# Kernel tuning notes

Hardware: AMD Instinct MI355X
Metric: run time of the kernel (lower is better)

The kernel has to match this reference:

```python
import jax, jax.numpy as jnp
import numpy as np

EMBED = 1024
HEADS = 16
HEAD_SIZE = EMBED // HEADS
B, T = 2, 2048
EPS = 1e-5


def layer_norm(x, g, b):
    mu = jnp.mean(x, axis=-1, keepdims=True)
    var = jnp.var(x, axis=-1, keepdims=True)
    return (x - mu) * jax.lax.rsqrt(var + EPS) * g + b


def setup_inputs() -> dict:
    key = jax.random.key(0)
    ks = jax.random.split(key, 12)
    s = 0.02
    return {
        "x": jax.random.normal(ks[0], (B, T, EMBED), jnp.float32),
        "Wq": s * jax.random.normal(ks[1], (EMBED, EMBED), jnp.float32),
        "Wk": s * jax.random.normal(ks[2], (EMBED, EMBED), jnp.float32),
        "Wv": s * jax.random.normal(ks[3], (EMBED, EMBED), jnp.float32),
        "Wo": s * jax.random.normal(ks[4], (EMBED, EMBED), jnp.float32),
        "bo": jnp.zeros((EMBED,), jnp.float32),
        "W1": s * jax.random.normal(ks[5], (EMBED, 4 * EMBED), jnp.float32),
        "b1": jnp.zeros((4 * EMBED,), jnp.float32),
        "W2": s * jax.random.normal(ks[6], (4 * EMBED, EMBED), jnp.float32),
        "b2": jnp.zeros((EMBED,), jnp.float32),
        "ln1_g": jnp.ones((EMBED,), jnp.float32),
        "ln1_b": jnp.zeros((EMBED,), jnp.float32),
        "ln2_g": jnp.ones((EMBED,), jnp.float32),
        "ln2_b": jnp.zeros((EMBED,), jnp.float32),
    }


def reference(x, Wq, Wk, Wv, Wo, bo, W1, b1, W2, b2, ln1_g, ln1_b, ln2_g, ln2_b):
    # --- multi-head causal self-attention on ln1(x) ---
    h = layer_norm(x, ln1_g, ln1_b)                      # [B,T,D]
    q = (h @ Wq).reshape(B, T, HEADS, HEAD_SIZE)         # per-head Q (concat layout)
    k = (h @ Wk).reshape(B, T, HEADS, HEAD_SIZE)
    v = (h @ Wv).reshape(B, T, HEADS, HEAD_SIZE)
    scores = jnp.einsum("bqhd,bkhd->bhqk", q, k) / jnp.sqrt(
        jnp.asarray(HEAD_SIZE, x.dtype)
    )                                                    # [B,H,T,T]
    causal = jnp.tril(jnp.ones((T, T), bool))
    scores = jnp.where(causal, scores, -jnp.inf)
    wei = jax.nn.softmax(scores, axis=-1)
    attn = jnp.einsum("bhqk,bkhd->bqhd", wei, v).reshape(B, T, EMBED)
    x = x + attn @ Wo + bo                               # residual (dropout=0)
    # --- feed-forward on ln2(x) ---
    h2 = layer_norm(x, ln2_g, ln2_b)
    ff = jax.nn.relu(h2 @ W1 + b1) @ W2 + b2
    return x + ff
```

## Files before the change

### kernel.cpp

```cpp
#include <hip/hip_runtime.h>


typedef __bf16 bf16;
typedef __attribute__((ext_vector_type(8))) __bf16 bf16x8;
typedef __attribute__((ext_vector_type(4))) __bf16 bf16x4;
typedef __attribute__((ext_vector_type(4))) short  shortx4;
typedef __attribute__((ext_vector_type(4))) float  floatx4;

__device__ __forceinline__ short f2bf_bits(float x) {
  return __builtin_bit_cast(short, (bf16)x);
}

__device__ __forceinline__ void gl2lds16(const bf16* g, bf16* l) {
  __builtin_amdgcn_global_load_lds((const __attribute__((address_space(1))) void*)g,
                                   (__attribute__((address_space(3))) void*)l, 16, 0, 0);
}

__device__ __forceinline__ void barx() {
  asm volatile("" ::: "memory");
  __builtin_amdgcn_s_barrier();
  asm volatile("" ::: "memory");
}

__global__ __launch_bounds__(256) void prep_kernel(
    const float* __restrict__ Wq, const float* __restrict__ Wk,
    const float* __restrict__ Wv, const float* __restrict__ Wo,
    const float* __restrict__ W1, const float* __restrict__ W2,
    bf16* __restrict__ WqkvT, bf16* __restrict__ WoT,
    bf16* __restrict__ W1T, bf16* __restrict__ W2T,
    const float* __restrict__ x, const float* __restrict__ ln1g,
    const float* __restrict__ ln1b, bf16* __restrict__ h1)
{
  int id = blockIdx.x;
  if (id >= 12288) {
    const int row = id - 12288, t = threadIdx.x;
    const float* xr = x + (size_t)row * 1024;
    float4 v = *(const float4*)(xr + t * 4);
    float s  = v.x + v.y + v.z + v.w;
    float s2 = v.x * v.x + v.y * v.y + v.z * v.z + v.w * v.w;
    #pragma unroll
    for (int off = 1; off < 64; off <<= 1) {
      s  += __shfl_xor(s, off);
      s2 += __shfl_xor(s2, off);
    }
    __shared__ float ps[4], ps2[4];
    int wv = t >> 6;
    if ((t & 63) == 0) { ps[wv] = s; ps2[wv] = s2; }
    __syncthreads();
    s  = ps[0] + ps[1] + ps[2] + ps[3];
    s2 = ps2[0] + ps2[1] + ps2[2] + ps2[3];
    const float mu = s * (1.0f / 1024.0f);
    const float rstd = rsqrtf(s2 * (1.0f / 1024.0f) - mu * mu + 1e-5f);
    float4 gv = *(const float4*)(ln1g + t * 4);
    float4 bv = *(const float4*)(ln1b + t * 4);
    bf16x4 o;
    o[0] = (bf16)((v.x - mu) * rstd * gv.x + bv.x);
    o[1] = (bf16)((v.y - mu) * rstd * gv.y + bv.y);
    o[2] = (bf16)((v.z - mu) * rstd * gv.z + bv.z);
    o[3] = (bf16)((v.w - mu) * rstd * gv.w + bv.w);
    *(bf16x4*)(h1 + (size_t)row * 1024 + t * 4) = o;
    return;
  }
  const float* src; bf16* dst; int K, N, tile;
  if (id < 4096) {
    K = 1024; N = 1024; tile = id & 1023;
    int wsel = id >> 10;
    src = (wsel == 0) ? Wq : (wsel == 1) ? Wk : (wsel == 2) ? Wv : Wo;
    dst = (wsel < 3) ? (WqkvT + (size_t)wsel * 1024 * 1024) : WoT;
  } else if (id < 8192) {
    K = 1024; N = 4096; tile = id - 4096; src = W1; dst = W1T;
  } else {
    K = 4096; N = 1024; tile = id - 8192; src = W2; dst = W2T;
  }
  int ntn = N >> 5;
  int k0 = (tile / ntn) * 32, n0 = (tile % ntn) * 32;
  __shared__ float tl[32][33];
  int tr = threadIdx.x >> 3, tc = (threadIdx.x & 7) * 4;
  float4 v = *(const float4*)(src + (size_t)(k0 + tr) * N + n0 + tc);
  tl[tr][tc + 0] = v.x; tl[tr][tc + 1] = v.y; tl[tr][tc + 2] = v.z; tl[tr][tc + 3] = v.w;
  __syncthreads();
  bf16x4 o = { (bf16)tl[tc + 0][tr], (bf16)tl[tc + 1][tr],
               (bf16)tl[tc + 2][tr], (bf16)tl[tc + 3][tr] };
  *(bf16x4*)(dst + (size_t)(n0 + tr) * K + k0 + tc) = o;
}

__device__ __forceinline__ void gemm_core(
    const bf16* __restrict__ A, const bf16* __restrict__ Bt,
    int Ktot, int k0, int k1, bf16* As, bf16* Bs, floatx4 (&acc)[4][4])
{
  const int tid = threadIdx.x, lane = tid & 63, wv = tid >> 6;
  const int li = lane & 15, g = lane >> 4;
  const int wm = wv >> 1, wn = wv & 1;
  const int srow = wv * 16 + (lane >> 2);
  const int scol = (lane & 3) * 8;
  const bf16* aP = A  + (size_t)srow * Ktot + scol;
  const bf16* bP = Bt + (size_t)srow * Ktot + scol;
  bf16* AsW = As + wv * 512;
  bf16* BsW = Bs + wv * 512;
  for (int kt = k0; kt < k1; kt += 64) {
    gl2lds16(aP + kt,                          AsW);
    gl2lds16(aP + kt + (size_t)64 * Ktot,      AsW + 2048);
    gl2lds16(aP + kt + 32,                     AsW + 4096);
    gl2lds16(aP + kt + 32 + (size_t)64 * Ktot, AsW + 6144);
    gl2lds16(bP + kt,                          BsW);
    gl2lds16(bP + kt + (size_t)64 * Ktot,      BsW + 2048);
    gl2lds16(bP + kt + 32,                     BsW + 4096);
    gl2lds16(bP + kt + 32 + (size_t)64 * Ktot, BsW + 6144);
    __syncthreads();
    #pragma unroll
    for (int hh = 0; hh < 2; ++hh) {
      const bf16* Ap = As + hh * 4096;
      const bf16* Bp = Bs + hh * 4096;
      bf16x8 af[4], bfr[4];
      #pragma unroll
      for (int r = 0; r < 4; ++r)
        af[r] = *(const bf16x8*)(Ap + (wm * 64 + r * 16 + li) * 32 + g * 8);
      #pragma unroll
      for (int c = 0; c < 4; ++c)
        bfr[c] = *(const bf16x8*)(Bp + (wn * 64 + c * 16 + li) * 32 + g * 8);
      #pragma unroll
      for (int r = 0; r < 4; ++r)
        #pragma unroll
        for (int c = 0; c < 4; ++c)
          acc[r][c] = __builtin_amdgcn_mfma_f32_16x16x32_bf16(bfr[c], af[r], acc[r][c], 0, 0, 0);
    }
    __syncthreads();
  }
}

__global__ __launch_bounds__(256) void gemm_splitk(
    const bf16* __restrict__ A, const bf16* __restrict__ Bt,
    bf16* __restrict__ Cp, int M, int N, int Ktot, int Kc)
{
  __shared__ bf16 As[8192];
  __shared__ bf16 Bs[8192];
  const int lane = threadIdx.x & 63, wv = threadIdx.x >> 6;
  const int li = lane & 15, g = lane >> 4;
  const int m0 = blockIdx.x * 128, n0 = blockIdx.y * 128;
  const int z = blockIdx.z;
  const int wm = wv >> 1, wn = wv & 1;
  floatx4 acc[4][4] = {};
  gemm_core(A + (size_t)m0 * Ktot, Bt + (size_t)n0 * Ktot, Ktot,
            z * Kc, (z + 1) * Kc, As, Bs, acc);
  bf16* C = Cp + (size_t)z * M * N;
  #pragma unroll
  for (int r = 0; r < 4; ++r) {
    int rowC = m0 + wm * 64 + r * 16 + li;
    #pragma unroll
    for (int c = 0; c < 4; ++c) {
      int colC = n0 + wn * 64 + c * 16 + g * 4;
      bf16x4 ov = { (bf16)acc[r][c][0], (bf16)acc[r][c][1],
                    (bf16)acc[r][c][2], (bf16)acc[r][c][3] };
      *(bf16x4*)(C + (size_t)rowC * N + colC) = ov;
    }
  }
}

#define MFMA_PHASE(RH, CH, BB)                                                  \
  do {                                                                          \
    __builtin_amdgcn_s_setprio(1);                                              \
    _Pragma("unroll") for (int ks = 0; ks < 2; ++ks)                            \
      _Pragma("unroll") for (int r = 0; r < 4; ++r)                             \
        _Pragma("unroll") for (int c = 0; c < 2; ++c)                           \
          acc[(RH) * 4 + r][(CH) * 2 + c] =                                     \
            __builtin_amdgcn_mfma_f32_16x16x32_bf16(                            \
                BB[c][ks], af[r][ks], acc[(RH) * 4 + r][(CH) * 2 + c], 0, 0, 0);\
    __builtin_amdgcn_s_setprio(0);                                              \
  } while (0)

__device__ __forceinline__ void gemm8_core(
    const bf16* __restrict__ A, const bf16* __restrict__ Bt,
    int K, int k0, int k1, bf16* lds, floatx4 (&acc)[8][4])
{
  const int lane = threadIdx.x & 63, wv = threadIdx.x >> 6;
  const int li = lane & 15, g = lane >> 4;
  const int wm2 = wv >> 2, wn4 = wv & 3;
  const int nt = (k1 - k0) >> 6;

  const int srow  = wv * 16 + (lane >> 3);
  const int schnk = ((lane & 7) ^ (lane >> 3)) * 8;
  const bf16* aSrc = A  + (size_t)srow * K + k0 + schnk;
  const bf16* bSrc = Bt + (size_t)srow * K + k0 + schnk;
  const size_t row8 = (size_t)8 * K;
  bf16* ldsB = lds + 32768;

  const int xk0 = ((0 + g) ^ (li & 7)) * 8;
  const int xk1 = ((4 + g) ^ (li & 7)) * 8;

  auto stA = [&](int t, int h) {
    if (t < nt) {
      const bf16* gp = aSrc + (size_t)(h * 128) * K + (t << 6);
      bf16* lp = lds + (((t & 1) * 2 + h) << 13) + wv * 1024;
      gl2lds16(gp, lp);
      gl2lds16(gp + row8, lp + 512);
    }
  };
  auto stB = [&](int t, int h) {
    if (t < nt) {
      const bf16* gp = bSrc + (size_t)(h * 128) * K + (t << 6);
      bf16* lp = ldsB + (((t & 1) * 2 + h) << 13) + wv * 1024;
      gl2lds16(gp, lp);
      gl2lds16(gp + row8, lp + 512);
    }
  };

  bf16x8 af[4][2], bA[2][2], bB[2][2];
  auto ldA = [&](int b, int RH) {
    const bf16* base = lds + ((b * 2 + RH) << 13) + (wm2 * 64 + li) * 64;
    #pragma unroll
    for (int r = 0; r < 4; ++r) {
      af[r][0] = *(const bf16x8*)(base + r * 1024 + xk0);
      af[r][1] = *(const bf16x8*)(base + r * 1024 + xk1);
    }
  };
  auto ldB = [&](int b, int CH, bf16x8 (&bb)[2][2]) {
    const bf16* base = ldsB + ((b * 2 + CH) << 13) + (wn4 * 32 + li) * 64;
    #pragma unroll
    for (int c = 0; c < 2; ++c) {
      bb[c][0] = *(const bf16x8*)(base + c * 1024 + xk0);
      bb[c][1] = *(const bf16x8*)(base + c * 1024 + xk1);
    }
  };

  stA(0, 0); stB(0, 0); stB(0, 1); stA(0, 1);
  stA(1, 0); stB(1, 0);
  asm volatile("s_waitcnt vmcnt(4)" ::: "memory");
  barx();

  for (int t = 0; t < nt; ++t) {
    const int b = t & 1;
    ldA(b, 0); ldB(b, 0, bA);
    stB(t + 1, 1);
    barx();
    MFMA_PHASE(0, 0, bA);
    barx();
    ldB(b, 1, bB);
    stA(t + 1, 1);
    asm volatile("s_waitcnt vmcnt(8)" ::: "memory");
    barx();
    MFMA_PHASE(0, 1, bB);
    barx();
    ldA(b, 1);
    stA(t + 2, 0);
    barx();
    MFMA_PHASE(1, 0, bA);
    barx();
    stB(t + 2, 0);
    asm volatile("s_waitcnt vmcnt(6)" ::: "memory");
    barx();
    MFMA_PHASE(1, 1, bB);
    barx();
  }
}

__device__ __forceinline__ void xcd_swz(int lin, int nwg, int nbx, int& bx, int& by) {
  int lin2 = (lin & 7) * (nwg >> 3) + (lin >> 3);
  bx = lin2 % nbx;
  by = lin2 / nbx;
}

__global__ __launch_bounds__(512, 2) void gemm8_ffn1(
    const bf16* __restrict__ A, const bf16* __restrict__ Bt,
    const float* __restrict__ bias, bf16* __restrict__ C,
    int M, int N, int K)
{
  __shared__ bf16 lds8[65536];
  int bx, by;
  xcd_swz(blockIdx.y * gridDim.x + blockIdx.x, gridDim.x * gridDim.y, gridDim.x, bx, by);
  const int m0 = bx * 256, n0 = by * 256;
  floatx4 acc[8][4] = {};
  gemm8_core(A + (size_t)m0 * K, Bt + (size_t)n0 * K, K, 0, K, lds8, acc);
  const int lane = threadIdx.x & 63, wv = threadIdx.x >> 6;
  const int li = lane & 15, g = lane >> 4;
  const int wm2 = wv >> 2, wn4 = wv & 3;
  #pragma unroll
  for (int ar = 0; ar < 8; ++ar) {
    int rowC = m0 + (ar >> 2) * 128 + wm2 * 64 + (ar & 3) * 16 + li;
    #pragma unroll
    for (int ac = 0; ac < 4; ++ac) {
      int colC = n0 + (ac >> 1) * 128 + wn4 * 32 + (ac & 1) * 16 + g * 4;
      float4 bv = *(const float4*)(bias + colC);
      bf16x4 ov = { (bf16)fmaxf(acc[ar][ac][0] + bv.x, 0.f),
                    (bf16)fmaxf(acc[ar][ac][1] + bv.y, 0.f),
                    (bf16)fmaxf(acc[ar][ac][2] + bv.z, 0.f),
                    (bf16)fmaxf(acc[ar][ac][3] + bv.w, 0.f) };
      *(bf16x4*)(C + (size_t)rowC * N + colC) = ov;
    }
  }
}

__global__ __launch_bounds__(512, 2) void gemm8_qkv(
    const bf16* __restrict__ A, const bf16* __restrict__ Bt,
    bf16* __restrict__ qkv, bf16* __restrict__ VtG)
{
  const int K = 1024;
  __shared__ bf16 lds8[65536];
  int bx, by;
  xcd_swz(blockIdx.y * gridDim.x + blockIdx.x, gridDim.x * gridDim.y, gridDim.x, bx, by);
  const int m0 = bx * 256, n0 = by * 256;
  floatx4 acc[8][4] = {};
  gemm8_core(A + (size_t)m0 * K, Bt + (size_t)n0 * K, K, 0, K, lds8, acc);
  const int lane = threadIdx.x & 63, wv = threadIdx.x >> 6;
  const int li = lane & 15, g = lane >> 4;
  const int wm2 = wv >> 2, wn4 = wv & 3;
  if (n0 < 2048) {
    #pragma unroll
    for (int ar = 0; ar < 8; ++ar) {
      int rowC = m0 + (ar >> 2) * 128 + wm2 * 64 + (ar & 3) * 16 + li;
      #pragma unroll
      for (int ac = 0; ac < 4; ++ac) {
        int colC = n0 + (ac >> 1) * 128 + wn4 * 32 + (ac & 1) * 16 + g * 4;
        bf16x4 ov = { (bf16)acc[ar][ac][0], (bf16)acc[ar][ac][1],
                      (bf16)acc[ar][ac][2], (bf16)acc[ar][ac][3] };
        *(bf16x4*)(qkv + (size_t)rowC * 3072 + colC) = ov;
      }
    }
  } else {
    #pragma unroll
    for (int ar = 0; ar < 8; ++ar) {
      int rowC = m0 + (ar >> 2) * 128 + wm2 * 64 + (ar & 3) * 16 + li;
      int key = rowC & 2047, bq = rowC >> 11;
      #pragma unroll
      for (int ac = 0; ac < 4; ++ac) {
        int vcol0 = n0 + (ac >> 1) * 128 + wn4 * 32 + (ac & 1) * 16 + g * 4 - 2048;
        #pragma unroll
        for (int e = 0; e < 4; ++e) {
          int vcol = vcol0 + e;
          int hh = vcol >> 6, d = vcol & 63;
          VtG[((size_t)(bq * 16 + hh) * 64 + d) * 2048 + key] = (bf16)acc[ar][ac][e];
        }
      }
    }
  }
}

__global__ __launch_bounds__(512, 2) void gemm8_splitk(
    const bf16* __restrict__ A, const bf16* __restrict__ Bt,
    bf16* __restrict__ Cp, int M, int N, int Ktot, int Kc)
{
  __shared__ bf16 lds8[65536];
  int bx, by;
  xcd_swz(blockIdx.y * gridDim.x + blockIdx.x, gridDim.x * gridDim.y, gridDim.x, bx, by);
  const int m0 = bx * 256, n0 = by * 256;
  const int z = blockIdx.z;
  floatx4 acc[8][4] = {};
  gemm8_core(A + (size_t)m0 * Ktot, Bt + (size_t)n0 * Ktot, Ktot,
             z * Kc, (z + 1) * Kc, lds8, acc);
  const int lane = threadIdx.x & 63, wv = threadIdx.x >> 6;
  const int li = lane & 15, g = lane >> 4;
  const int wm2 = wv >> 2, wn4 = wv & 3;
  bf16* C = Cp + (size_t)z * M * N;
  #pragma unroll
  for (int ar = 0; ar < 8; ++ar) {
    int rowC = m0 + (ar >> 2) * 128 + wm2 * 64 + (ar & 3) * 16 + li;
    #pragma unroll
    for (int ac = 0; ac < 4; ++ac) {
      int colC = n0 + (ac >> 1) * 128 + wn4 * 32 + (ac & 1) * 16 + g * 4;
      bf16x4 ov = { (bf16)acc[ar][ac][0], (bf16)acc[ar][ac][1],
                    (bf16)acc[ar][ac][2], (bf16)acc[ar][ac][3] };
      *(bf16x4*)(C + (size_t)rowC * N + colC) = ov;
    }
  }
}

__global__ __launch_bounds__(256) void combine_wo_ln2(
    const bf16* __restrict__ P, const float* __restrict__ bo,
    const float* __restrict__ x, const float* __restrict__ gam,
    const float* __restrict__ bet, float* __restrict__ x2, bf16* __restrict__ h2)
{
  const int row = blockIdx.x, t = threadIdx.x;
  const size_t base = (size_t)row * 1024 + t * 4;
  float4 v = *(const float4*)(x + base);
  bf16x4 p0 = *(const bf16x4*)(P + base);
  bf16x4 p1 = *(const bf16x4*)(P + 4194304 + base);
  float4 bv = *(const float4*)(bo + t * 4);
  v.x += (float)p0[0] + (float)p1[0] + bv.x;
  v.y += (float)p0[1] + (float)p1[1] + bv.y;
  v.z += (float)p0[2] + (float)p1[2] + bv.z;
  v.w += (float)p0[3] + (float)p1[3] + bv.w;
  *(float4*)(x2 + base) = v;
  float s  = v.x + v.y + v.z + v.w;
  float s2 = v.x * v.x + v.y * v.y + v.z * v.z + v.w * v.w;
  #pragma unroll
  for (int off = 1; off < 64; off <<= 1) {
    s  += __shfl_xor(s, off);
    s2 += __shfl_xor(s2, off);
  }
  __shared__ float ps[4], ps2[4];
  int wv = t >> 6;
  if ((t & 63) == 0) { ps[wv] = s; ps2[wv] = s2; }
  __syncthreads();
  s  = ps[0] + ps[1] + ps[2] + ps[3];
  s2 = ps2[0] + ps2[1] + ps2[2] + ps2[3];
  const float mu = s * (1.0f / 1024.0f);
  const float rstd = rsqrtf(s2 * (1.0f / 1024.0f) - mu * mu + 1e-5f);
  float4 gv = *(const float4*)(gam + t * 4);
  float4 bb = *(const float4*)(bet + t * 4);
  bf16x4 o;
  o[0] = (bf16)((v.x - mu) * rstd * gv.x + bb.x);
  o[1] = (bf16)((v.y - mu) * rstd * gv.y + bb.y);
  o[2] = (bf16)((v.z - mu) * rstd * gv.z + bb.z);
  o[3] = (bf16)((v.w - mu) * rstd * gv.w + bb.w);
  *(bf16x4*)(h2 + base) = o;
}

__global__ __launch_bounds__(256) void combine_ffn2(
    const bf16* __restrict__ P, const float* __restrict__ b2,
    const float* __restrict__ x2, float* __restrict__ out)
{
  const size_t i = ((size_t)blockIdx.x * 256 + threadIdx.x) * 4;
  const int col = (int)(i & 1023);
  float4 acc = *(const float4*)(x2 + i);
  float4 bv = *(const float4*)(b2 + col);
  acc.x += bv.x; acc.y += bv.y; acc.z += bv.z; acc.w += bv.w;
  #pragma unroll
  for (int z = 0; z < 4; ++z) {
    bf16x4 p = *(const bf16x4*)(P + (size_t)z * 4194304 + i);
    acc.x += (float)p[0]; acc.y += (float)p[1];
    acc.z += (float)p[2]; acc.w += (float)p[3];
  }
  *(float4*)(out + i) = acc;
}

__global__ __launch_bounds__(256, 2) void attn_kernel(
    const bf16* __restrict__ qkv, const bf16* __restrict__ VtG,
    bf16* __restrict__ attnb)
{
  __shared__ bf16 Ks[2][128 * 72];
  __shared__ bf16 Vt[2][64 * 136];
  const int t = threadIdx.x, lane = t & 63, wv = t >> 6;
  const int li = lane & 15, g = lane >> 4;
  const int xl = blockIdx.x & 7;
  const int r_ = blockIdx.x >> 3;
  const int g2 = r_ & 3, p = r_ >> 2;
  const int bh = g2 * 8 + xl;
  const int b = bh >> 4, h = bh & 15;
  const int row0 = b << 11;
  const int tlo = p * 4 + wv, thi = 127 - tlo;
  const int q0l = tlo << 4, q0h = thi << 4;
  const size_t qkvbase = (size_t)row0 * 3072 + (size_t)h * 64;
  const bf16* vgbase = VtG + (size_t)(b * 16 + h) * 64 * 2048;

  const bf16* qpl = qkv + qkvbase + (size_t)(q0l + li) * 3072 + g * 8;
  const bf16* qph = qkv + qkvbase + (size_t)(q0h + li) * 3072 + g * 8;
  bf16x8 bl0 = *(const bf16x8*)(qpl), bl1 = *(const bf16x8*)(qpl + 32);
  bf16x8 bh0 = *(const bf16x8*)(qph), bh1 = *(const bf16x8*)(qph + 32);

  floatx4 ol[4] = {}, oh[4] = {};
  float ll = 0.f, lh = 0.f;
  const int cmax = 31 - p;
  const int CC = (cmax + 2) >> 1;

  const int krow0 = t >> 3, kdc = (t & 7) * 8;
  const int vd = t >> 2, vkg = (t & 3) * 16;
  bf16x8 kv0, kv1, kv2, kv3, vv0, vv1, vv2, vv3;

  auto ld = [&](int cc) {
    const size_t kb = qkvbase + (size_t)(cc * 128) * 3072 + 1024;
    kv0 = *(const bf16x8*)(qkv + kb + (size_t)(krow0     ) * 3072 + kdc);
    kv1 = *(const bf16x8*)(qkv + kb + (size_t)(krow0 + 32) * 3072 + kdc);
    kv2 = *(const bf16x8*)(qkv + kb + (size_t)(krow0 + 64) * 3072 + kdc);
    kv3 = *(const bf16x8*)(qkv + kb + (size_t)(krow0 + 96) * 3072 + kdc);
    const bf16* vg = vgbase + (size_t)vd * 2048 + cc * 128 + vkg;
    vv0 = *(const bf16x8*)(vg);
    vv1 = *(const bf16x8*)(vg + 8);
    vv2 = *(const bf16x8*)(vg + 64);
    vv3 = *(const bf16x8*)(vg + 72);
  };
  auto wr = [&](int buf) {
    *(bf16x8*)(Ks[buf] + (krow0     ) * 72 + kdc) = kv0;
    *(bf16x8*)(Ks[buf] + (krow0 + 32) * 72 + kdc) = kv1;
    *(bf16x8*)(Ks[buf] + (krow0 + 64) * 72 + kdc) = kv2;
    *(bf16x8*)(Ks[buf] + (krow0 + 96) * 72 + kdc) = kv3;
    *(bf16x8*)(Vt[buf] + vd * 136 + vkg)      = vv0;
    *(bf16x8*)(Vt[buf] + vd * 136 + vkg + 8)  = vv1;
    *(bf16x8*)(Vt[buf] + vd * 136 + vkg + 64) = vv2;
    *(bf16x8*)(Vt[buf] + vd * 136 + vkg + 72) = vv3;
  };

  auto proc = [&](const bf16* KsB, const bf16* VtB, int h64,
                  const bf16x8& bq0, const bf16x8& bq1, float& l_i,
                  floatx4 (&o)[4], int qg, int k0, bool diag) {
    floatx4 sv[4];
    #pragma unroll
    for (int s = 0; s < 4; ++s) {
      const bf16* kr = KsB + (h64 * 64 + s * 16 + li) * 72 + g * 8;
      bf16x8 a0 = *(const bf16x8*)(kr);
      bf16x8 a1 = *(const bf16x8*)(kr + 32);
      floatx4 z = {0.f, 0.f, 0.f, 0.f};
      z = __builtin_amdgcn_mfma_f32_16x16x32_bf16(a0, bq0, z, 0, 0, 0);
      z = __builtin_amdgcn_mfma_f32_16x16x32_bf16(a1, bq1, z, 0, 0, 0);
      sv[s] = z;
    }
    float pv[4][4];
    float rs = 0.f;
    #pragma unroll
    for (int s = 0; s < 4; ++s)
      #pragma unroll
      for (int e = 0; e < 4; ++e) {
        float val = __expf(sv[s][e] * 0.125f - 4.0f);
        if (diag) {
          int kg = k0 + s * 16 + g * 4 + e;
          val = (kg <= qg) ? val : 0.0f;
        }
        pv[s][e] = val;
        rs += val;
      }
    rs += __shfl_xor(rs, 16);
    rs += __shfl_xor(rs, 32);
    l_i += rs;
    #pragma unroll
    for (int s = 0; s < 4; ++s) {
      shortx4 bp = { f2bf_bits(pv[s][0]), f2bf_bits(pv[s][1]),
                     f2bf_bits(pv[s][2]), f2bf_bits(pv[s][3]) };
      #pragma unroll
      for (int c = 0; c < 4; ++c) {
        shortx4 av = *(const shortx4*)(VtB + (c * 16 + li) * 136 + h64 * 64 + s * 16 + g * 4);
        o[c] = __builtin_amdgcn_mfma_f32_16x16x16bf16_1k(av, bp, o[c], 0, 0, 0);
      }
    }
  };

  ld(0);
  wr(0);
  __syncthreads();
  int buf = 0;
  for (int cc = 0; cc < CC; ++cc) {
    if (cc + 1 < CC) ld(cc + 1);
    const int c0 = cc * 2, c1 = c0 + 1;
    proc(Ks[buf], Vt[buf], 0, bh0, bh1, lh, oh, q0h + li, c0 * 64, c0 == cmax);
    if (c0 <= p) proc(Ks[buf], Vt[buf], 0, bl0, bl1, ll, ol, q0l + li, c0 * 64, c0 == p);
    if (c1 <= cmax) {
      proc(Ks[buf], Vt[buf], 1, bh0, bh1, lh, oh, q0h + li, c1 * 64, c1 == cmax);
      if (c1 <= p) proc(Ks[buf], Vt[buf], 1, bl0, bl1, ll, ol, q0l + li, c1 * 64, c1 == p);
    }
    if (cc + 1 < CC) wr(buf ^ 1);
    __syncthreads();
    buf ^= 1;
  }

  const float invh = 1.0f / lh, invl = 1.0f / ll;
  #pragma unroll
  for (int c = 0; c < 4; ++c) {
    bf16x4 ovh = { (bf16)(oh[c][0] * invh), (bf16)(oh[c][1] * invh),
                   (bf16)(oh[c][2] * invh), (bf16)(oh[c][3] * invh) };
    *(bf16x4*)(attnb + (size_t)(row0 + q0h + li) * 1024 + h * 64 + c * 16 + g * 4) = ovh;
    bf16x4 ovl = { (bf16)(ol[c][0] * invl), (bf16)(ol[c][1] * invl),
                   (bf16)(ol[c][2] * invl), (bf16)(ol[c][3] * invl) };
    *(bf16x4*)(attnb + (size_t)(row0 + q0l + li) * 1024 + h * 64 + c * 16 + g * 4) = ovl;
  }
}

extern "C" void kernel_launch(void* const* d_in, const int* in_sizes, int n_in,
                              void* d_out, int out_size, void* d_ws, size_t ws_size,
                              hipStream_t stream) {
  (void)in_sizes; (void)n_in; (void)out_size; (void)ws_size;
  const float* x    = (const float*)d_in[0];
  const float* Wq   = (const float*)d_in[1];
  const float* Wk   = (const float*)d_in[2];
  const float* Wv   = (const float*)d_in[3];
  const float* Wo   = (const float*)d_in[4];
  const float* bo   = (const float*)d_in[5];
  const float* W1   = (const float*)d_in[6];
  const float* b1   = (const float*)d_in[7];
  const float* W2   = (const float*)d_in[8];
  const float* b2   = (const float*)d_in[9];
  const float* ln1g = (const float*)d_in[10];
  const float* ln1b = (const float*)d_in[11];
  const float* ln2g = (const float*)d_in[12];
  const float* ln2b = (const float*)d_in[13];
  float* out = (float*)d_out;
  char* ws = (char*)d_ws;

  constexpr size_t OFF_WQKVT = 0;
  constexpr size_t OFF_WOT   = OFF_WQKVT + 3072ull * 1024 * 2;
  constexpr size_t OFF_W1T   = OFF_WOT   + 1024ull * 1024 * 2;
  constexpr size_t OFF_W2T   = OFF_W1T   + 4096ull * 1024 * 2;
  constexpr size_t OFF_H1    = OFF_W2T   + 1024ull * 4096 * 2;
  constexpr size_t OFF_QKV   = OFF_H1    + 4096ull * 1024 * 2;
  constexpr size_t OFF_ATT   = OFF_QKV   + 4096ull * 3072 * 2;
  constexpr size_t OFF_X2    = OFF_ATT   + 4096ull * 1024 * 2;
  constexpr size_t OFF_H2    = OFF_X2    + 4096ull * 1024 * 4;
  constexpr size_t OFF_F1    = OFF_H2    + 4096ull * 1024 * 2;
  constexpr size_t OFF_PART  = OFF_F1    + 4096ull * 4096 * 2;
  constexpr size_t OFF_VTG   = OFF_PART  + 4ull * 4096 * 1024 * 2;

  bf16*  WqkvT = (bf16*)(ws + OFF_WQKVT);
  bf16*  WoT   = (bf16*)(ws + OFF_WOT);
  bf16*  W1T   = (bf16*)(ws + OFF_W1T);
  bf16*  W2T   = (bf16*)(ws + OFF_W2T);
  bf16*  h1    = (bf16*)(ws + OFF_H1);
  bf16*  qkv   = (bf16*)(ws + OFF_QKV);
  bf16*  attnb = (bf16*)(ws + OFF_ATT);
  float* x2    = (float*)(ws + OFF_X2);
  bf16*  h2    = (bf16*)(ws + OFF_H2);
  bf16*  f1    = (bf16*)(ws + OFF_F1);
  bf16*  part  = (bf16*)(ws + OFF_PART);
  bf16*  vtg   = (bf16*)(ws + OFF_VTG);

  prep_kernel<<<16384, 256, 0, stream>>>(Wq, Wk, Wv, Wo, W1, W2,
                                         WqkvT, WoT, W1T, W2T, x, ln1g, ln1b, h1);
  gemm8_qkv<<<dim3(16, 12), 512, 0, stream>>>(h1, WqkvT, qkv, vtg);
  attn_kernel<<<512, 256, 0, stream>>>(qkv, vtg, attnb);
  gemm_splitk<<<dim3(32, 8, 2), 256, 0, stream>>>(attnb, WoT, part, 4096, 1024, 1024, 512);
  combine_wo_ln2<<<4096, 256, 0, stream>>>(part, bo, x, ln2g, ln2b, x2, h2);
  gemm8_ffn1<<<dim3(16, 16), 512, 0, stream>>>(h2, W1T, b1, f1, 4096, 4096, 1024);
  gemm8_splitk<<<dim3(16, 4, 4), 512, 0, stream>>>(f1, W2T, part, 4096, 1024, 4096, 1024);
  combine_ffn2<<<4096, 256, 0, stream>>>(part, b2, x2, out);
}
```

Measured before the change: 320.4 us.

## Read K and V directly from global memory in attention, dropping LDS staging

Removes the double-buffered shared-memory staging of K and V tiles and the per-chunk block barriers in the attention kernel. Each wave now loads its MFMA operands for K and transposed V straight from global memory, relying on L1/L2 caching. This removes LDS traffic and synchronisation, but raises global load traffic and latency with no software prefetch, and the four waves redundantly fetch the same K/V rows.

```diff
diff --git a/kernel.cpp b/kernel.cpp
--- a/kernel.cpp
+++ b/kernel.cpp
@@ -426,8 +426,6 @@
     const bf16* __restrict__ qkv, const bf16* __restrict__ VtG,
     bf16* __restrict__ attnb)
 {
-  __shared__ bf16 Ks[2][128 * 72];
-  __shared__ bf16 Vt[2][64 * 136];
   const int t = threadIdx.x, lane = t & 63, wv = t >> 6;
   const int li = lane & 15, g = lane >> 4;
   const int xl = blockIdx.x & 7;
@@ -440,6 +438,7 @@
   const int q0l = tlo << 4, q0h = thi << 4;
   const size_t qkvbase = (size_t)row0 * 3072 + (size_t)h * 64;
   const bf16* vgbase = VtG + (size_t)(b * 16 + h) * 64 * 2048;
+  const bf16* kbase  = qkv + qkvbase + 1024;
 
   const bf16* qpl = qkv + qkvbase + (size_t)(q0l + li) * 3072 + g * 8;
   const bf16* qph = qkv + qkvbase + (size_t)(q0h + li) * 3072 + g * 8;
@@ -449,42 +448,20 @@
   floatx4 ol[4] = {}, oh[4] = {};
   float ll = 0.f, lh = 0.f;
   const int cmax = 31 - p;
-  const int CC = (cmax + 2) >> 1;
-
-  const int krow0 = t >> 3, kdc = (t & 7) * 8;
-  const int vd = t >> 2, vkg = (t & 3) * 16;
-  bf16x8 kv0, kv1, kv2, kv3, vv0, vv1, vv2, vv3;
-
-  auto ld = [&](int cc) {
-    const size_t kb = qkvbase + (size_t)(cc * 128) * 3072 + 1024;
-    kv0 = *(const bf16x8*)(qkv + kb + (size_t)(krow0     ) * 3072 + kdc);
-    kv1 = *(const bf16x8*)(qkv + kb + (size_t)(krow0 + 32) * 3072 + kdc);
-    kv2 = *(const bf16x8*)(qkv + kb + (size_t)(krow0 + 64) * 3072 + kdc);
-    kv3 = *(const bf16x8*)(qkv + kb + (size_t)(krow0 + 96) * 3072 + kdc);
-    const bf16* vg = vgbase + (size_t)vd * 2048 + cc * 128 + vkg;
-    vv0 = *(const bf16x8*)(vg);
-    vv1 = *(const bf16x8*)(vg + 8);
-    vv2 = *(const bf16x8*)(vg + 64);
-    vv3 = *(const bf16x8*)(vg + 72);
-  };
-  auto wr = [&](int buf) {
-    *(bf16x8*)(Ks[buf] + (krow0     ) * 72 + kdc) = kv0;
-    *(bf16x8*)(Ks[buf] + (krow0 + 32) * 72 + kdc) = kv1;
-    *(bf16x8*)(Ks[buf] + (krow0 + 64) * 72 + kdc) = kv2;
-    *(bf16x8*)(Ks[buf] + (krow0 + 96) * 72 + kdc) = kv3;
-    *(bf16x8*)(Vt[buf] + vd * 136 + vkg)      = vv0;
-    *(bf16x8*)(Vt[buf] + vd * 136 + vkg + 8)  = vv1;
-    *(bf16x8*)(Vt[buf] + vd * 136 + vkg + 64) = vv2;
-    *(bf16x8*)(Vt[buf] + vd * 136 + vkg + 72) = vv3;
-  };
-
-  auto proc = [&](const bf16* KsB, const bf16* VtB, int h64,
-                  const bf16x8& bq0, const bf16x8& bq1, float& l_i,
-                  floatx4 (&o)[4], int qg, int k0, bool diag) {
+
+  const bf16* krow = kbase + (size_t)li * 3072 + g * 8;
+  const bf16* vrow[4];
+  #pragma unroll
+  for (int co = 0; co < 4; ++co)
+    vrow[co] = vgbase + (size_t)(co * 16 + li) * 2048 + g * 4;
+
+  auto proc = [&](int c, const bf16x8& bq0, const bf16x8& bq1, float& l_i,
+                  floatx4 (&o)[4], int qg, bool diag) {
+    const bf16* kc = krow + (size_t)(c * 64) * 3072;
     floatx4 sv[4];
     #pragma unroll
     for (int s = 0; s < 4; ++s) {
-      const bf16* kr = KsB + (h64 * 64 + s * 16 + li) * 72 + g * 8;
+      const bf16* kr = kc + (size_t)(s * 16) * 3072;
       bf16x8 a0 = *(const bf16x8*)(kr);
       bf16x8 a1 = *(const bf16x8*)(kr + 32);
       floatx4 z = {0.f, 0.f, 0.f, 0.f};
@@ -500,7 +477,7 @@
       for (int e = 0; e < 4; ++e) {
         float val = __expf(sv[s][e] * 0.125f - 4.0f);
         if (diag) {
-          int kg = k0 + s * 16 + g * 4 + e;
+          int kg = c * 64 + s * 16 + g * 4 + e;
           val = (kg <= qg) ? val : 0.0f;
         }
         pv[s][e] = val;
@@ -514,29 +491,16 @@
       shortx4 bp = { f2bf_bits(pv[s][0]), f2bf_bits(pv[s][1]),
                      f2bf_bits(pv[s][2]), f2bf_bits(pv[s][3]) };
       #pragma unroll
-      for (int c = 0; c < 4; ++c) {
-        shortx4 av = *(const shortx4*)(VtB + (c * 16 + li) * 136 + h64 * 64 + s * 16 + g * 4);
-        o[c] = __builtin_amdgcn_mfma_f32_16x16x16bf16_1k(av, bp, o[c], 0, 0, 0);
+      for (int co = 0; co < 4; ++co) {
+        shortx4 av = *(const shortx4*)(vrow[co] + c * 64 + s * 16);
+        o[co] = __builtin_amdgcn_mfma_f32_16x16x16bf16_1k(av, bp, o[co], 0, 0, 0);
       }
     }
   };
 
-  ld(0);
-  wr(0);
-  __syncthreads();
-  int buf = 0;
-  for (int cc = 0; cc < CC; ++cc) {
-    if (cc + 1 < CC) ld(cc + 1);
-    const int c0 = cc * 2, c1 = c0 + 1;
-    proc(Ks[buf], Vt[buf], 0, bh0, bh1, lh, oh, q0h + li, c0 * 64, c0 == cmax);
-    if (c0 <= p) proc(Ks[buf], Vt[buf], 0, bl0, bl1, ll, ol, q0l + li, c0 * 64, c0 == p);
-    if (c1 <= cmax) {
-      proc(Ks[buf], Vt[buf], 1, bh0, bh1, lh, oh, q0h + li, c1 * 64, c1 == cmax);
-      if (c1 <= p) proc(Ks[buf], Vt[buf], 1, bl0, bl1, ll, ol, q0l + li, c1 * 64, c1 == p);
-    }
-    if (cc + 1 < CC) wr(buf ^ 1);
-    __syncthreads();
-    buf ^= 1;
+  for (int c = 0; c <= cmax; ++c) {
+    proc(c, bh0, bh1, lh, oh, q0h + li, c == cmax);
+    if (c <= p) proc(c, bl0, bl1, ll, ol, q0l + li, c == p);
   }
 
   const float invh = 1.0f / lh, invl = 1.0f / ll;
```

Result: slower. 428.5 us (+33.7%).
